# Kernel tuning notes

Measured on AMD Instinct MI355X. Metric: run time of the kernel, lower is better.

## Reference

```python
import jax, jax.numpy as jnp
import numpy as np

B, S, E = 2, 2048, 2048
H, KV, D = 32, 8, 128
EPS = 1e-6


def _rope_tables(seq_len, head_dim, base=1_000_000.0):
    inv_freq = 1.0 / (base ** (np.arange(0, head_dim, 2, dtype=np.float32) / head_dim))
    ang = np.arange(seq_len, dtype=np.float32)[:, None] * inv_freq[None, :]  # [S, D/2]
    cos = np.concatenate([np.cos(ang), np.cos(ang)], axis=-1)  # [S, D]
    sin = np.concatenate([np.sin(ang), np.sin(ang)], axis=-1)
    return jnp.asarray(cos), jnp.asarray(sin)


def setup_inputs() -> dict:
    key = jax.random.key(0)
    ks = jax.random.split(key, 8)
    x = jax.random.normal(ks[0], (B, S, E), dtype=jnp.float32)
    mask = jnp.triu(jnp.ones((S, S), dtype=bool), k=1)  # True = masked (causal)
    cos, sin = _rope_tables(S, D)
    w = 0.02
    Wq = jax.random.normal(ks[1], (E, H * D), dtype=jnp.float32) * w
    bq = jnp.zeros((H * D,), dtype=jnp.float32)
    Wk = jax.random.normal(ks[2], (E, KV * D), dtype=jnp.float32) * w
    bk = jnp.zeros((KV * D,), dtype=jnp.float32)
    Wv = jax.random.normal(ks[3], (E, KV * D), dtype=jnp.float32) * w
    bv = jnp.zeros((KV * D,), dtype=jnp.float32)
    Wo = jax.random.normal(ks[4], (H * D, E), dtype=jnp.float32) * w
    q_scale = jnp.ones((D,), dtype=jnp.float32)
    k_scale = jnp.ones((D,), dtype=jnp.float32)
    return {"x": x, "mask": mask, "cos": cos, "sin": sin, "Wq": Wq, "bq": bq,
            "Wk": Wk, "bk": bk, "Wv": Wv, "bv": bv, "Wo": Wo,
            "q_scale": q_scale, "k_scale": k_scale}


def _rmsnorm(x, scale):
    xf = x.astype(jnp.float32)
    var = jnp.mean(xf * xf, axis=-1, keepdims=True)
    return (xf * jax.lax.rsqrt(var + EPS) * scale).astype(x.dtype)


def _apply_rope(x, cos, sin):
    # x: [B, h, S, D]; cos/sin: [S, D]
    d2 = x.shape[-1] // 2
    x1, x2 = x[..., :d2], x[..., d2:]
    rotated = jnp.concatenate([-x2, x1], axis=-1)
    return (x * cos[None, None] + rotated * sin[None, None]).astype(x.dtype)


def reference(x, mask, cos, sin, Wq, bq, Wk, bk, Wv, bv, Wo, q_scale, k_scale):
    b, s, _ = x.shape
    q = (x @ Wq + bq).reshape(b, s, H, D).transpose(0, 2, 1, 3)   # [B,H,S,D]
    k = (x @ Wk + bk).reshape(b, s, KV, D).transpose(0, 2, 1, 3)  # [B,KV,S,D]
    v = (x @ Wv + bv).reshape(b, s, KV, D).transpose(0, 2, 1, 3)
    q = _rmsnorm(q, q_scale)
    k = _rmsnorm(k, k_scale)
    q = _apply_rope(q, cos, sin)
    k = _apply_rope(k, cos, sin)
    group = H // KV
    k = jnp.repeat(k, group, axis=1)  # repeat_interleave on head dim -> [B,H,S,D]
    v = jnp.repeat(v, group, axis=1)
    scores = jnp.einsum("bhqd,bhkd->bhqk", q, k)
    scores = jnp.where(mask[None, None], -jnp.inf, scores)
    attn = jax.nn.softmax(scores / jnp.sqrt(jnp.float32(D)), axis=-1)
    ctx = jnp.einsum("bhqk,bhkd->bhqd", attn, v)
    ctx = ctx.transpose(0, 2, 1, 3).reshape(b, s, H * D)
    return ctx @ Wo
```

## Files before the change

### kernel.cpp

```cpp
#include <hip/hip_runtime.h>

typedef short short8 __attribute__((ext_vector_type(8)));
typedef float f32x4 __attribute__((ext_vector_type(4)));
typedef float f32x16 __attribute__((ext_vector_type(16)));
typedef unsigned int uint2v __attribute__((ext_vector_type(2)));

static __device__ __forceinline__ ushort f2bf(float f){
  union { float f; uint u; } cv; cv.f = f;
  uint u = cv.u;
  uint r = (u + 0x7fffu + ((u >> 16) & 1u)) >> 16;
  return (ushort)r;
}
static __device__ __forceinline__ float bf2f(ushort h){
  union { uint u; float f; } cv; cv.u = ((uint)h) << 16; return cv.f;
}
static __device__ __forceinline__ f32x4 mfma16x16x32(short8 a, short8 b, f32x4 c){
  return __builtin_amdgcn_mfma_f32_16x16x32_bf16(a, b, c, 0, 0, 0);
}
static __device__ __forceinline__ f32x16 mfma32(short8 a, short8 b, f32x16 c){
  return __builtin_amdgcn_mfma_f32_32x32x16_bf16(a, b, c, 0, 0, 0);
}
static __device__ __forceinline__ float ex2(float x){
  float r; asm("v_exp_f32 %0, %1" : "=v"(r) : "v"(x)); return r;
}
static __device__ __forceinline__ uint cvtpk(float lo, float hi){
  uint r; asm("v_cvt_pk_bf16_f32 %0, %1, %2" : "=v"(r) : "v"(lo), "v"(hi)); return r;
}
static __device__ __forceinline__ void glds16(const void* g, const void* l){
  __builtin_amdgcn_global_load_lds((const __attribute__((address_space(1))) void*)g,
                                   (__attribute__((address_space(3))) void*)l, 16, 0, 0);
}
static __device__ __forceinline__ void store_out(float* p, float v){ *p = v; }
static __device__ __forceinline__ void store_out(ushort* p, float v){ *p = f2bf(v); }

__global__ void cvt_bf16_kernel(const float* __restrict__ x, ushort* __restrict__ y, int n4){
  int i = blockIdx.x * 256 + threadIdx.x;
  if (i < n4){
    float4 v = reinterpret_cast<const float4*>(x)[i];
    ushort4 o; o.x = f2bf(v.x); o.y = f2bf(v.y); o.z = f2bf(v.z); o.w = f2bf(v.w);
    reinterpret_cast<ushort4*>(y)[i] = o;
  }
}

__global__ void transpose_cvt_kernel(const float* __restrict__ W, ushort* __restrict__ WT, int K, int N){
  __shared__ float tile[32][33];
  int n0 = blockIdx.x * 32, k0 = blockIdx.y * 32;
  int tx = threadIdx.x, ty = threadIdx.y;
  #pragma unroll
  for (int i = 0; i < 4; i++){ int r = ty + i * 8; tile[r][tx] = W[(size_t)(k0 + r) * N + n0 + tx]; }
  __syncthreads();
  #pragma unroll
  for (int i = 0; i < 4; i++){ int r = ty + i * 8; WT[(size_t)(n0 + r) * K + k0 + tx] = f2bf(tile[tx][r]); }
}

__global__ void bias_concat_kernel(const float* __restrict__ bq, const float* __restrict__ bk,
                                   const float* __restrict__ bv, float* __restrict__ out){
  int i = blockIdx.x * 256 + threadIdx.x;
  if (i < 6144) out[i] = (i < 4096) ? bq[i] : ((i < 5120) ? bk[i - 4096] : bv[i - 5120]);
}

template<typename OutT>
__global__ __launch_bounds__(256) void gemm_bt_kernel(const ushort* __restrict__ A, const ushort* __restrict__ BT,
                                                      const float* __restrict__ bias, OutT* __restrict__ C,
                                                      int M, int N, int K){
  __shared__ ushort As[128 * 32];
  __shared__ ushort Bs[128 * 32];
  const int m0 = blockIdx.y * 128, n0 = blockIdx.x * 128;
  const int tid = threadIdx.x, w = tid >> 6, l = tid & 63, lm = l & 15, lk = l >> 4;
  const int wr = w >> 1, wc = w & 1;
  const int srow0 = (w * 64 + l) >> 2, srow1 = 64 + srow0;
  const int sseg  = l & 3;
  const int sw0 = sseg ^ ((srow0 >> 1) & 3), sw1 = sseg ^ ((srow1 >> 1) & 3);
  const int rchunk = lk ^ ((lm >> 1) & 3);
  const size_t aoff0 = (size_t)(m0 + srow0) * K + sw0 * 8;
  const size_t aoff1 = (size_t)(m0 + srow1) * K + sw1 * 8;
  const size_t boff0 = (size_t)(n0 + srow0) * K + sw0 * 8;
  const size_t boff1 = (size_t)(n0 + srow1) * K + sw1 * 8;
  ushort* dstA0 = &As[(w * 64) * 8];
  ushort* dstA1 = &As[(256 + w * 64) * 8];
  ushort* dstB0 = &Bs[(w * 64) * 8];
  ushort* dstB1 = &Bs[(256 + w * 64) * 8];
  f32x4 acc[4][4] = {};
  for (int k0 = 0; k0 < K; k0 += 32){
    __syncthreads();
    glds16(A  + aoff0 + k0, dstA0);
    glds16(A  + aoff1 + k0, dstA1);
    glds16(BT + boff0 + k0, dstB0);
    glds16(BT + boff1 + k0, dstB1);
    __syncthreads();
    short8 af[4], bfr[4];
    #pragma unroll
    for (int mi = 0; mi < 4; mi++) af[mi]  = *(const short8*)&As[(wr * 64 + mi * 16 + lm) * 32 + rchunk * 8];
    #pragma unroll
    for (int ni = 0; ni < 4; ni++) bfr[ni] = *(const short8*)&Bs[(wc * 64 + ni * 16 + lm) * 32 + rchunk * 8];
    #pragma unroll
    for (int mi = 0; mi < 4; mi++)
      #pragma unroll
      for (int ni = 0; ni < 4; ni++)
        acc[mi][ni] = mfma16x16x32(af[mi], bfr[ni], acc[mi][ni]);
  }
  #pragma unroll
  for (int mi = 0; mi < 4; mi++)
    #pragma unroll
    for (int ni = 0; ni < 4; ni++){
      int col = n0 + wc * 64 + ni * 16 + lm;
      float bb = bias ? bias[col] : 0.0f;
      #pragma unroll
      for (int r = 0; r < 4; r++){
        int row = m0 + wr * 64 + mi * 16 + lk * 4 + r;
        store_out(&C[(size_t)row * N + col], acc[mi][ni][r] + bb);
      }
    }
}

#define QSCL2 0.12752016f
__global__ __launch_bounds__(256) void norm_rope_kernel(const ushort* __restrict__ qkv,
    const float* __restrict__ cosT, const float* __restrict__ sinT,
    const float* __restrict__ qs, const float* __restrict__ ksc,
    ushort* __restrict__ qo, ushort* __restrict__ ko, ushort* __restrict__ vto){
  int slot = blockIdx.x * 4 + (threadIdx.x >> 6);
  int lane = threadIdx.x & 63;
  int row = slot / 48, c = slot % 48;
  int b = row >> 11, s = row & 2047;
  size_t base = (size_t)row * 6144 + c * 128;
  float e1 = bf2f(qkv[base + lane]);
  float e2 = bf2f(qkv[base + lane + 64]);
  if (c < 40){
    float ss = e1 * e1 + e2 * e2;
    #pragma unroll
    for (int m = 1; m < 64; m <<= 1) ss += __shfl_xor(ss, m);
    float rs = rsqrtf(ss * (1.0f / 128.0f) + 1e-6f);
    const float* sc = (c < 32) ? qs : ksc;
    float n1 = e1 * rs * sc[lane], n2 = e2 * rs * sc[lane + 64];
    float c1 = cosT[s * 128 + lane],      s1 = sinT[s * 128 + lane];
    float c2 = cosT[s * 128 + lane + 64], s2 = sinT[s * 128 + lane + 64];
    float o1 = n1 * c1 - n2 * s1;
    float o2 = n2 * c2 + n1 * s2;
    if (c < 32){
      size_t ob = ((size_t)(b * 32 + c) * 2048 + s) * 128;
      qo[ob + lane] = f2bf(o1 * QSCL2); qo[ob + lane + 64] = f2bf(o2 * QSCL2);
    } else {
      int kv = c - 32;
      size_t ob = ((size_t)(b * 8 + kv) * 2048 + s) * 128;
      ko[ob + lane] = f2bf(o1); ko[ob + lane + 64] = f2bf(o2);
    }
  } else {
    int kv = c - 40;
    size_t ob = (size_t)(b * 8 + kv) * 128;
    vto[(ob + lane) * 2048 + s]      = f2bf(e1);
    vto[(ob + lane + 64) * 2048 + s] = f2bf(e2);
  }
}

__global__ __launch_bounds__(256, 2) void flash_kernel(const ushort* __restrict__ Q, const ushort* __restrict__ Kg,
    const ushort* __restrict__ VTg, ushort* __restrict__ ctx){
  __shared__ ushort Kl[64 * 128];
  __shared__ ushort Vl[128 * 64];
  const int bh = blockIdx.y, b = bh >> 5, h = bh & 31, kvh = h >> 2;
  const int qb = gridDim.x - 1 - blockIdx.x;
  const int q0 = qb * 128;
  const int tid = threadIdx.x, w = tid >> 6, l = tid & 63;
  const int q31 = l & 31, hi = l >> 5, swz = q31 & 7;
  const int qw = q0 + w * 32;
  const int myq = qw + q31;
  const ushort* Kbase = Kg  + (size_t)(b * 8 + kvh) * 2048 * 128;
  const ushort* Vbase = VTg + (size_t)(b * 8 + kvh) * 128 * 2048;
  const ushort* Qp = Q + ((size_t)(b * 32 + h) * 2048 + myq) * 128;
  short8 qf[8];
  #pragma unroll
  for (int s = 0; s < 8; s++) qf[s] = *(const short8*)(Qp + s * 16 + hi * 8);
  f32x16 o[4] = {};
  float m_r = -INFINITY, l_r = 0.f;
  const int krow = l >> 4, kcol = l & 15;
  const int vrow = l >> 3, vcol = l & 7;
  const int nt = 2 * qb + 2;
  for (int kt = 0; kt < nt; kt++){
    __syncthreads();
    #pragma unroll
    for (int i2 = 0; i2 < 4; i2++){
      int i = w * 4 + i2;
      int row = i * 4 + krow;
      glds16(Kbase + (size_t)(kt * 64 + row) * 128 + ((kcol ^ (row & 7)) * 8), &Kl[i * 512]);
    }
    #pragma unroll
    for (int j2 = 0; j2 < 4; j2++){
      int j = w * 4 + j2;
      int row = j * 8 + vrow;
      glds16(Vbase + (size_t)row * 2048 + kt * 64 + ((vcol ^ (row & 7)) * 8), &Vl[j * 512]);
    }
    __syncthreads();
    f32x16 sa0 = {}, sa1 = {};
    __builtin_amdgcn_s_setprio(1);
    #pragma unroll
    for (int s = 0; s < 8; s++){
      short8 a0 = *(const short8*)&Kl[q31 * 128 + (((2 * s + hi) ^ swz) * 8)];
      short8 a1 = *(const short8*)&Kl[(32 + q31) * 128 + (((2 * s + hi) ^ swz) * 8)];
      sa0 = mfma32(a0, qf[s], sa0);
      sa1 = mfma32(a1, qf[s], sa1);
    }
    __builtin_amdgcn_s_setprio(0);
    if (kt >= 2 * qb){
      #pragma unroll
      for (int r = 0; r < 16; r++){
        int krel = (r & 3) + 8 * (r >> 2) + 4 * hi;
        if (kt * 64 + krel > myq)      sa0[r] = -INFINITY;
        if (kt * 64 + 32 + krel > myq) sa1[r] = -INFINITY;
      }
    }
    float mx = fmaxf(sa0[0], sa1[0]);
    #pragma unroll
    for (int r = 1; r < 16; r++) mx = fmaxf(mx, fmaxf(sa0[r], sa1[r]));
    mx = fmaxf(mx, __shfl_xor(mx, 32));
    if (!__all(mx - m_r <= 8.f)){
      float mn = fmaxf(m_r, mx);
      float al = ex2(m_r - mn);
      m_r = mn; l_r *= al;
      #pragma unroll
      for (int r = 0; r < 16; r++){
        float alq = __shfl(al, (r & 3) + 8 * (r >> 2) + 4 * hi);
        o[0][r] *= alq; o[1][r] *= alq; o[2][r] *= alq; o[3][r] *= alq;
      }
    }
    float rsum = 0.f;
    #pragma unroll
    for (int r = 0; r < 16; r++){
      sa0[r] = ex2(sa0[r] - m_r);
      sa1[r] = ex2(sa1[r] - m_r);
      rsum += sa0[r] + sa1[r];
    }
    rsum += __shfl_xor(rsum, 32);
    l_r += rsum;
    uint pk0[8], pk1[8];
    #pragma unroll
    for (int t = 0; t < 8; t++){
      pk0[t] = cvtpk(sa0[2 * t], sa0[2 * t + 1]);
      pk1[t] = cvtpk(sa1[2 * t], sa1[2 * t + 1]);
    }
    __builtin_amdgcn_s_setprio(1);
    #pragma unroll
    for (int sub = 0; sub < 2; sub++){
      #pragma unroll
      for (int kc = 0; kc < 2; kc++){
        uint p0 = sub ? pk1[4 * kc]     : pk0[4 * kc];
        uint p1 = sub ? pk1[4 * kc + 1] : pk0[4 * kc + 1];
        uint p2 = sub ? pk1[4 * kc + 2] : pk0[4 * kc + 2];
        uint p3 = sub ? pk1[4 * kc + 3] : pk0[4 * kc + 3];
        uint2v r02 = __builtin_amdgcn_permlane32_swap(p0, p2, false, false);
        uint2v r13 = __builtin_amdgcn_permlane32_swap(p1, p3, false, false);
        union { uint u[4]; short8 v; } Af;
        Af.u[0] = r02[0]; Af.u[1] = r13[0]; Af.u[2] = r02[1]; Af.u[3] = r13[1];
        #pragma unroll
        for (int dc = 0; dc < 4; dc++){
          short8 vf = *(const short8*)&Vl[(dc * 32 + q31) * 64 + (((4 * sub + 2 * kc + hi) ^ swz) * 8)];
          o[dc] = mfma32(Af.v, vf, o[dc]);
        }
      }
    }
    __builtin_amdgcn_s_setprio(0);
  }
  float invl = 1.0f / l_r;
  ushort* Cp = ctx + (size_t)(b * 2048 + qw) * 4096 + (size_t)h * 128;
  #pragma unroll
  for (int r = 0; r < 16; r++){
    int qrel = (r & 3) + 8 * (r >> 2) + 4 * hi;
    float inv = __shfl(invl, qrel);
    #pragma unroll
    for (int dc = 0; dc < 4; dc++)
      Cp[(size_t)qrel * 4096 + dc * 32 + q31] = f2bf(o[dc][r] * inv);
  }
}

extern "C" void kernel_launch(void* const* d_in, const int* in_sizes, int n_in,
                              void* d_out, int out_size, void* d_ws, size_t ws_size,
                              hipStream_t stream){
  const float* x    = (const float*)d_in[0];
  const float* cosT = (const float*)d_in[2];
  const float* sinT = (const float*)d_in[3];
  const float* Wq   = (const float*)d_in[4];
  const float* bq   = (const float*)d_in[5];
  const float* Wk   = (const float*)d_in[6];
  const float* bk   = (const float*)d_in[7];
  const float* Wv   = (const float*)d_in[8];
  const float* bv   = (const float*)d_in[9];
  const float* Wo   = (const float*)d_in[10];
  const float* qs   = (const float*)d_in[11];
  const float* ksc  = (const float*)d_in[12];
  float* out = (float*)d_out;
  char* ws = (char*)d_ws;

  ushort* xb    = (ushort*)(ws + 0);
  ushort* wtqkv = (ushort*)(ws + 16777216);
  float*  biasq = (float* )(ws + 41943040);
  ushort* qkv   = (ushort*)(ws + 41967616);
  ushort* qb_   = (ushort*)(ws + 92299264);
  ushort* kb_   = (ushort*)(ws + 125853696);
  ushort* vtb   = (ushort*)(ws + 134242304);
  ushort* ctx   = (ushort*)(ws + 142630912);
  ushort* wot   = (ushort*)(ws + 176185344);

  cvt_bf16_kernel<<<8192, 256, 0, stream>>>(x, xb, 2097152);
  transpose_cvt_kernel<<<dim3(128, 64), dim3(32, 8), 0, stream>>>(Wq, wtqkv, 2048, 4096);
  transpose_cvt_kernel<<<dim3(32, 64),  dim3(32, 8), 0, stream>>>(Wk, wtqkv + (size_t)4096 * 2048, 2048, 1024);
  transpose_cvt_kernel<<<dim3(32, 64),  dim3(32, 8), 0, stream>>>(Wv, wtqkv + (size_t)5120 * 2048, 2048, 1024);
  transpose_cvt_kernel<<<dim3(64, 128), dim3(32, 8), 0, stream>>>(Wo, wot, 4096, 2048);
  bias_concat_kernel<<<24, 256, 0, stream>>>(bq, bk, bv, biasq);

  gemm_bt_kernel<ushort><<<dim3(48, 32), 256, 0, stream>>>(xb, wtqkv, biasq, qkv, 4096, 6144, 2048);
  norm_rope_kernel<<<49152, 256, 0, stream>>>(qkv, cosT, sinT, qs, ksc, qb_, kb_, vtb);
  flash_kernel<<<dim3(16, 64), 256, 0, stream>>>(qb_, kb_, vtb, ctx);
  gemm_bt_kernel<float><<<dim3(16, 32), 256, 0, stream>>>(ctx, wot, nullptr, out, 4096, 2048, 4096);
}
```

Baseline: 472.9 us.

## Double-buffer K/V tiles in flash attention and swizzle GEMM blocks across XCDs

The flash kernel now keeps two LDS buffers for K and V. It issues the global-to-LDS loads for the next tile before computing the current one and uses vmcnt waits plus barriers to order the buffers, so memory latency overlaps with MFMA work. Separately, the GEMM remaps workgroup IDs so consecutive tiles land on the same XCD, which should improve L2 reuse. The double buffer doubles LDS use to 64KB per block, which may conflict with the 2-blocks-per-CU launch bound. The hand-counted vmcnt(8) has to match the issue order exactly.

```diff
diff --git a/kernel.cpp b/kernel.cpp
--- a/kernel.cpp
+++ b/kernel.cpp
@@ -32,6 +32,11 @@
 }
 static __device__ __forceinline__ void store_out(float* p, float v){ *p = v; }
 static __device__ __forceinline__ void store_out(ushort* p, float v){ *p = f2bf(v); }
+static __device__ __forceinline__ int xcd_swizzle(int flat, int nwg){
+  int q = nwg >> 3, r = nwg & 7;
+  int xcd = flat & 7, idx = flat >> 3;
+  return (xcd < r) ? xcd * (q + 1) + idx : r * (q + 1) + (xcd - r) * q + idx;
+}
 
 __global__ void cvt_bf16_kernel(const float* __restrict__ x, ushort* __restrict__ y, int n4){
   int i = blockIdx.x * 256 + threadIdx.x;
@@ -65,7 +70,9 @@
                                                       int M, int N, int K){
   __shared__ ushort As[128 * 32];
   __shared__ ushort Bs[128 * 32];
-  const int m0 = blockIdx.y * 128, n0 = blockIdx.x * 128;
+  const int nwg = gridDim.x * gridDim.y;
+  const int wg = xcd_swizzle(blockIdx.y * gridDim.x + blockIdx.x, nwg);
+  const int m0 = (wg / gridDim.x) * 128, n0 = (wg % gridDim.x) * 128;
   const int tid = threadIdx.x, w = tid >> 6, l = tid & 63, lm = l & 15, lk = l >> 4;
   const int wr = w >> 1, wc = w & 1;
   const int srow0 = (w * 64 + l) >> 2, srow1 = 64 + srow0;
@@ -154,8 +161,8 @@
 
 __global__ __launch_bounds__(256, 2) void flash_kernel(const ushort* __restrict__ Q, const ushort* __restrict__ Kg,
     const ushort* __restrict__ VTg, ushort* __restrict__ ctx){
-  __shared__ ushort Kl[64 * 128];
-  __shared__ ushort Vl[128 * 64];
+  __shared__ ushort Kl[2][64 * 128];
+  __shared__ ushort Vl[2][128 * 64];
   const int bh = blockIdx.y, b = bh >> 5, h = bh & 31, kvh = h >> 2;
   const int qb = gridDim.x - 1 - blockIdx.x;
   const int q0 = qb * 128;
@@ -174,27 +181,39 @@
   const int krow = l >> 4, kcol = l & 15;
   const int vrow = l >> 3, vcol = l & 7;
   const int nt = 2 * qb + 2;
+
+  #define STAGE(KT, BS) do {                                                            \
+    _Pragma("unroll")                                                                   \
+    for (int i2 = 0; i2 < 4; i2++){                                                     \
+      int i = w * 4 + i2; int row = i * 4 + krow;                                       \
+      glds16(Kbase + (size_t)((KT) * 64 + row) * 128 + ((kcol ^ (row & 7)) * 8),        \
+             &Kl[BS][i * 512]);                                                         \
+    }                                                                                   \
+    _Pragma("unroll")                                                                   \
+    for (int j2 = 0; j2 < 4; j2++){                                                     \
+      int j = w * 4 + j2; int row = j * 8 + vrow;                                       \
+      glds16(Vbase + (size_t)row * 2048 + (KT) * 64 + ((vcol ^ (row & 7)) * 8),         \
+             &Vl[BS][j * 512]);                                                         \
+    }                                                                                   \
+  } while (0)
+
+  STAGE(0, 0);
   for (int kt = 0; kt < nt; kt++){
-    __syncthreads();
-    #pragma unroll
-    for (int i2 = 0; i2 < 4; i2++){
-      int i = w * 4 + i2;
-      int row = i * 4 + krow;
-      glds16(Kbase + (size_t)(kt * 64 + row) * 128 + ((kcol ^ (row & 7)) * 8), &Kl[i * 512]);
-    }
-    #pragma unroll
-    for (int j2 = 0; j2 < 4; j2++){
-      int j = w * 4 + j2;
-      int row = j * 8 + vrow;
-      glds16(Vbase + (size_t)row * 2048 + kt * 64 + ((vcol ^ (row & 7)) * 8), &Vl[j * 512]);
-    }
-    __syncthreads();
+    const int cur = kt & 1;
+    if (kt + 1 < nt){
+      STAGE(kt + 1, cur ^ 1);
+      asm volatile("s_waitcnt vmcnt(8)" ::: "memory");
+    } else {
+      asm volatile("s_waitcnt vmcnt(0)" ::: "memory");
+    }
+    __builtin_amdgcn_s_barrier();
+    asm volatile("" ::: "memory");
     f32x16 sa0 = {}, sa1 = {};
     __builtin_amdgcn_s_setprio(1);
     #pragma unroll
     for (int s = 0; s < 8; s++){
-      short8 a0 = *(const short8*)&Kl[q31 * 128 + (((2 * s + hi) ^ swz) * 8)];
-      short8 a1 = *(const short8*)&Kl[(32 + q31) * 128 + (((2 * s + hi) ^ swz) * 8)];
+      short8 a0 = *(const short8*)&Kl[cur][q31 * 128 + (((2 * s + hi) ^ swz) * 8)];
+      short8 a1 = *(const short8*)&Kl[cur][(32 + q31) * 128 + (((2 * s + hi) ^ swz) * 8)];
       sa0 = mfma32(a0, qf[s], sa0);
       sa1 = mfma32(a1, qf[s], sa1);
     }
@@ -251,13 +270,16 @@
         Af.u[0] = r02[0]; Af.u[1] = r13[0]; Af.u[2] = r02[1]; Af.u[3] = r13[1];
         #pragma unroll
         for (int dc = 0; dc < 4; dc++){
-          short8 vf = *(const short8*)&Vl[(dc * 32 + q31) * 64 + (((4 * sub + 2 * kc + hi) ^ swz) * 8)];
+          short8 vf = *(const short8*)&Vl[cur][(dc * 32 + q31) * 64 + (((4 * sub + 2 * kc + hi) ^ swz) * 8)];
           o[dc] = mfma32(Af.v, vf, o[dc]);
         }
       }
     }
     __builtin_amdgcn_s_setprio(0);
-  }
+    asm volatile("" ::: "memory");
+    __builtin_amdgcn_s_barrier();
+  }
+  #undef STAGE
   float invl = 1.0f / l_r;
   ushort* Cp = ctx + (size_t)(b * 2048 + qw) * 4096 + (size_t)h * 128;
   #pragma unroll
```

Result: slower. 491.4 us (+3.9%).
